# Optimization experiments

Hardware: AMD Instinct MI355X
Metric: run time of the kernel (lower is better)

Reference implementation:

```python
import jax, jax.numpy as jnp
import numpy as np

N_NODES = 100000
N_EDGES = 800000
D_MODEL = 128


def setup_inputs() -> dict:
    key = jax.random.key(0)
    ks = jax.random.split(key, 8)
    nodes = jax.random.normal(ks[0], (N_NODES, D_MODEL), dtype=jnp.float32)
    senders = jax.random.randint(ks[1], (N_EDGES,), 0, N_NODES)
    receivers = jax.random.randint(ks[2], (N_EDGES,), 0, N_NODES)
    edges = jax.random.uniform(ks[3], (N_EDGES,), dtype=jnp.float32)
    W1 = jax.random.normal(ks[4], (D_MODEL, D_MODEL), dtype=jnp.float32) / np.sqrt(D_MODEL)
    b1 = jnp.zeros((D_MODEL,), dtype=jnp.float32)
    W2 = jax.random.normal(ks[5], (D_MODEL, D_MODEL), dtype=jnp.float32) / np.sqrt(D_MODEL)
    b2 = jnp.zeros((D_MODEL,), dtype=jnp.float32)
    return {"nodes": nodes, "senders": senders, "receivers": receivers,
            "edges": edges, "W1": W1, "b1": b1, "W2": W2, "b2": b2}


def _gcn_conv(x, s, r, e, W, b):
    # GCNConv (add_self_loops=False): linear transform, symmetric degree
    # normalization by edge weights, scatter-add aggregation at receivers.
    x = x @ W  # [N, d]
    deg = jax.ops.segment_sum(e, r, num_segments=N_NODES)  # weighted in-degree [N]
    dis = jnp.where(deg > 0, jax.lax.rsqrt(jnp.where(deg > 0, deg, 1.0)), 0.0)
    w = dis[s] * e * dis[r]  # normalized edge weight [E]
    msg = x[s] * w[:, None]  # gather + scale, [E, d] (dominant HBM traffic)
    out = jax.ops.segment_sum(msg, r, num_segments=N_NODES)  # scatter-add [N, d]
    return out + b


def reference(nodes, senders, receivers, edges, W1, b1, W2, b2):
    # to_undirected: duplicate every edge in both directions
    s = jnp.concatenate([senders, receivers])
    r = jnp.concatenate([receivers, senders])
    e = jnp.concatenate([edges, edges])
    # k_hop = 2 with residual (tightening_factor == 1), no activation, no norm
    nodes = nodes + _gcn_conv(nodes, s, r, e, W1, b1)
    nodes = nodes + _gcn_conv(nodes, s, r, e, W2, b2)
    return nodes
```

## Files before the change

### kernel.cpp

```cpp
#include <hip/hip_runtime.h>
#include <hip/hip_bf16.h>

#define D 128

typedef __attribute__((ext_vector_type(8))) short bf16x8;
typedef __attribute__((ext_vector_type(4))) float f32x4;

static __device__ __forceinline__ short f2bf(float f) {
  __hip_bfloat16 h = __float2bfloat16(f);
  return *reinterpret_cast<short*>(&h);
}

__global__ __launch_bounds__(256) void k_degcnt(
    const int* __restrict__ s, const int* __restrict__ r,
    const float* __restrict__ e, float* __restrict__ deg,
    int* __restrict__ cnt, int E) {
  int i = blockIdx.x * 256 + threadIdx.x;
  if (i < E) {
    int sv = s[i], rv = r[i];
    float ev = e[i];
    atomicAdd(&deg[rv], ev);
    atomicAdd(&deg[sv], ev);
    atomicAdd(&cnt[rv], 1);
    atomicAdd(&cnt[sv], 1);
  }
}

__global__ __launch_bounds__(256) void k_dis(float* __restrict__ deg, int N) {
  int i = blockIdx.x * 256 + threadIdx.x;
  if (i < N) {
    float d = deg[i];
    deg[i] = d > 0.f ? rsqrtf(d) : 0.f;
  }
}

__global__ __launch_bounds__(256) void k_scan1(
    const int* __restrict__ cnt, int* __restrict__ rowptr,
    int* __restrict__ chsum, int N) {
  __shared__ int ts[256];
  int tid = threadIdx.x;
  int base = blockIdx.x * 2048 + tid * 8;
  int v[8];
  int run = 0;
#pragma unroll
  for (int j = 0; j < 8; ++j) {
    int idx = base + j;
    int t = (idx < N) ? cnt[idx] : 0;
    v[j] = run;
    run += t;
  }
  ts[tid] = run;
  __syncthreads();
  for (int off = 1; off < 256; off <<= 1) {
    int t = (tid >= off) ? ts[tid - off] : 0;
    __syncthreads();
    ts[tid] += t;
    __syncthreads();
  }
  int excl = ts[tid] - run;
#pragma unroll
  for (int j = 0; j < 8; ++j) {
    int idx = base + j;
    if (idx < N) rowptr[idx] = excl + v[j];
  }
  if (tid == 255) chsum[blockIdx.x] = ts[255];
}

__global__ __launch_bounds__(64) void k_scan2(int* __restrict__ chsum, int nch) {
  if (threadIdx.x == 0) {
    int run = 0;
    for (int i = 0; i < nch; ++i) { int t = chsum[i]; chsum[i] = run; run += t; }
    chsum[nch] = run;
  }
}

__global__ __launch_bounds__(256) void k_scan3(
    int* __restrict__ rowptr, int* __restrict__ cursor,
    const int* __restrict__ chsum, int N, int nch) {
  int i = blockIdx.x * 256 + threadIdx.x;
  if (i < N) {
    int v = rowptr[i] + chsum[i >> 11];
    rowptr[i] = v;
    cursor[i] = v;
  } else if (i == N) {
    rowptr[N] = chsum[nch];
  }
}

__global__ __launch_bounds__(256) void k_fill(
    const int* __restrict__ s, const int* __restrict__ r,
    const float* __restrict__ e, const float* __restrict__ dis,
    int* __restrict__ cursor, int2* __restrict__ ent, int E) {
  int i = blockIdx.x * 256 + threadIdx.x;
  if (i >= E) return;
  int sv = s[i], rv = r[i];
  float w = dis[sv] * e[i] * dis[rv];
  int wy = __float_as_int(w);
  int p1 = atomicAdd(&cursor[rv], 1);
  ent[p1] = make_int2(sv, wy);
  int p2 = atomicAdd(&cursor[sv], 1);
  ent[p2] = make_int2(rv, wy);
}

__global__ __launch_bounds__(256) void k_wprep2(
    const float* __restrict__ W1, const float* __restrict__ W2,
    unsigned short* __restrict__ Wt1, unsigned short* __restrict__ Wt2) {
  int idx = blockIdx.x * 256 + threadIdx.x;
  const float* W = (idx < D * D) ? W1 : W2;
  unsigned short* Wt = (idx < D * D) ? Wt1 : Wt2;
  int t = idx & (D * D - 1);
  int col = t >> 7, k = t & 127;
  Wt[t] = (unsigned short)f2bf(W[k * D + col]);
}

__global__ __launch_bounds__(256) void k_gemm_mfma(
    const float* __restrict__ X, const unsigned short* __restrict__ Wt,
    unsigned short* __restrict__ Y, int nrows) {
  __shared__ unsigned short wl[128 * 128];
  int tid = threadIdx.x;
  {
    const int4* src = reinterpret_cast<const int4*>(Wt);
#pragma unroll
    for (int j = 0; j < 8; ++j) {
      int c = tid + 256 * j;
      int4 v = src[c];
      int byte = c * 16;
      int col = byte >> 8;
      int swz = byte ^ ((col & 7) << 4);
      *reinterpret_cast<int4*>(reinterpret_cast<char*>(wl) + swz) = v;
    }
  }
  __syncthreads();

  int lane = tid & 63;
  int wv = tid >> 6;
  int lr = lane & 15;
  int kgrp = lane >> 4;
  int row = blockIdx.x * 64 + wv * 16 + lr;
  bool valid = row < nrows;

  f32x4 acc[8];
#pragma unroll
  for (int n = 0; n < 8; ++n) acc[n] = (f32x4){0.f, 0.f, 0.f, 0.f};

#pragma unroll
  for (int ks = 0; ks < 4; ++ks) {
    bf16x8 a;
    if (valid) {
      const float4* xp = reinterpret_cast<const float4*>(
          X + (size_t)row * D + ks * 32 + kgrp * 8);
      float4 f0 = xp[0], f1 = xp[1];
      a[0] = f2bf(f0.x); a[1] = f2bf(f0.y); a[2] = f2bf(f0.z); a[3] = f2bf(f0.w);
      a[4] = f2bf(f1.x); a[5] = f2bf(f1.y); a[6] = f2bf(f1.z); a[7] = f2bf(f1.w);
    } else {
      a = (bf16x8){0, 0, 0, 0, 0, 0, 0, 0};
    }
#pragma unroll
    for (int n = 0; n < 8; ++n) {
      int col = n * 16 + lr;
      int byte = col * 256 + ks * 64 + kgrp * 16;
      int swz = byte ^ ((col & 7) << 4);
      bf16x8 b = *reinterpret_cast<const bf16x8*>(
          reinterpret_cast<const char*>(wl) + swz);
      acc[n] = __builtin_amdgcn_mfma_f32_16x16x32_bf16(a, b, acc[n], 0, 0, 0);
    }
  }

  int r0 = blockIdx.x * 64 + wv * 16 + kgrp * 4;
#pragma unroll
  for (int n = 0; n < 8; ++n) {
    int col = n * 16 + lr;
#pragma unroll
    for (int i = 0; i < 4; ++i) {
      int rr = r0 + i;
      if (rr < nrows) Y[(size_t)rr * D + col] = (unsigned short)f2bf(acc[n][i]);
    }
  }
}

__global__ __launch_bounds__(256) void k_agg(
    const int* __restrict__ rowptr, const int2* __restrict__ ent,
    const unsigned int* __restrict__ X2, const float* __restrict__ prev,
    const float* __restrict__ bias, float* __restrict__ out, int N) {
  int node = blockIdx.x * 4 + (threadIdx.x >> 6);
  int lane = threadIdx.x & 63;
  if (node >= N) return;
  float2 acc = reinterpret_cast<const float2*>(prev)[(size_t)node * 64 + lane];
  float2 bb = reinterpret_cast<const float2*>(bias)[lane];
  acc.x += bb.x; acc.y += bb.y;
  int beg = rowptr[node], end = rowptr[node + 1];
  int j = beg;
  for (; j + 8 <= end; j += 8) {
    int2 ee[8];
#pragma unroll
    for (int u = 0; u < 8; ++u) ee[u] = ent[j + u];
    unsigned int xz[8];
#pragma unroll
    for (int u = 0; u < 8; ++u) xz[u] = X2[(size_t)ee[u].x * 64 + lane];
#pragma unroll
    for (int u = 0; u < 8; ++u) {
      float w = __int_as_float(ee[u].y);
      acc.x = fmaf(__uint_as_float(xz[u] << 16), w, acc.x);
      acc.y = fmaf(__uint_as_float(xz[u] & 0xffff0000u), w, acc.y);
    }
  }
  for (; j < end; ++j) {
    int2 eJ = ent[j];
    float w = __int_as_float(eJ.y);
    unsigned int xz = X2[(size_t)eJ.x * 64 + lane];
    acc.x = fmaf(__uint_as_float(xz << 16), w, acc.x);
    acc.y = fmaf(__uint_as_float(xz & 0xffff0000u), w, acc.y);
  }
  reinterpret_cast<float2*>(out)[(size_t)node * 64 + lane] = acc;
}

extern "C" void kernel_launch(void* const* d_in, const int* in_sizes, int n_in,
                              void* d_out, int out_size, void* d_ws, size_t ws_size,
                              hipStream_t stream) {
  const float* nodes     = (const float*)d_in[0];
  const int*   senders   = (const int*)d_in[1];
  const int*   receivers = (const int*)d_in[2];
  const float* edges     = (const float*)d_in[3];
  const float* W1        = (const float*)d_in[4];
  const float* b1        = (const float*)d_in[5];
  const float* W2        = (const float*)d_in[6];
  const float* b2        = (const float*)d_in[7];
  float* out = (float*)d_out;

  int N = in_sizes[0] / D;
  int E = in_sizes[1];
  int NCH = (N + 2047) / 2048;

  auto alignup = [](size_t x) { return (x + 511) / 512 * 512; };
  char* p = (char*)d_ws;
  float* deg    = (float*)p; p += alignup((size_t)N * 4);
  int*   cnt    = (int*)p;   p += alignup((size_t)N * 4);
  int*   rowptr = (int*)p;   p += alignup(((size_t)N + 1) * 4);
  int*   cursor = (int*)p;   p += alignup((size_t)N * 4);
  int*   chsum  = (int*)p;   p += alignup(((size_t)NCH + 1) * 4);
  int2*  ent    = (int2*)p;  p += alignup((size_t)2 * E * 8);
  unsigned short* Wt1 = (unsigned short*)p; p += alignup((size_t)D * D * 2);
  unsigned short* Wt2 = (unsigned short*)p; p += alignup((size_t)D * D * 2);
  unsigned short* X   = (unsigned short*)p;

  hipMemsetAsync(deg, 0, (size_t)N * 4, stream);
  hipMemsetAsync(cnt, 0, (size_t)N * 4, stream);

  int eb = (E + 255) / 256;
  k_degcnt<<<eb, 256, 0, stream>>>(senders, receivers, edges, deg, cnt, E);
  k_dis<<<(N + 255) / 256, 256, 0, stream>>>(deg, N);

  k_scan1<<<NCH, 256, 0, stream>>>(cnt, rowptr, chsum, N);
  k_scan2<<<1, 64, 0, stream>>>(chsum, NCH);
  k_scan3<<<(N + 1 + 255) / 256, 256, 0, stream>>>(rowptr, cursor, chsum, N, NCH);
  k_fill<<<eb, 256, 0, stream>>>(senders, receivers, edges, deg, cursor, ent, E);

  k_wprep2<<<(2 * D * D) / 256, 256, 0, stream>>>(W1, W2, Wt1, Wt2);

  int gemm_blocks = (N + 63) / 64;
  int agg_blocks = (N + 3) / 4;

  k_gemm_mfma<<<gemm_blocks, 256, 0, stream>>>(nodes, Wt1, X, N);
  k_agg<<<agg_blocks, 256, 0, stream>>>(rowptr, ent, (const unsigned int*)X,
                                        nodes, b1, out, N);

  k_gemm_mfma<<<gemm_blocks, 256, 0, stream>>>(out, Wt2, X, N);
  k_agg<<<agg_blocks, 256, 0, stream>>>(rowptr, ent, (const unsigned int*)X,
                                        out, b2, out, N);
}
```

Baseline: 533.5 us.

## Compute degrees from CSR rows instead of float atomics; add nontemporal hints

Removes the float atomic degree accumulation and the per-node rsqrt pass. Edges are now bucketed with their raw weights, then each node's degree is summed from its CSR row with a wave reduction, and a second per-row pass rewrites the weights into normalized form. Nontemporal loads and stores are also added for the edge streams, the CSR fill, and the aggregation prev/out rows. This trades 1.6M float atomics for two extra passes over the 12.8MB CSR. The nontemporal stores of out may also hurt reuse when the second GEMM reads that buffer.

```diff
diff --git a/kernel.cpp b/kernel.cpp
--- a/kernel.cpp
+++ b/kernel.cpp
@@ -5,32 +5,23 @@
 
 typedef __attribute__((ext_vector_type(8))) short bf16x8;
 typedef __attribute__((ext_vector_type(4))) float f32x4;
+typedef __attribute__((ext_vector_type(2))) float f32x2;
+typedef __attribute__((ext_vector_type(2))) int int2v;
 
 static __device__ __forceinline__ short f2bf(float f) {
   __hip_bfloat16 h = __float2bfloat16(f);
   return *reinterpret_cast<short*>(&h);
 }
 
-__global__ __launch_bounds__(256) void k_degcnt(
+__global__ __launch_bounds__(256) void k_cnt(
     const int* __restrict__ s, const int* __restrict__ r,
-    const float* __restrict__ e, float* __restrict__ deg,
     int* __restrict__ cnt, int E) {
   int i = blockIdx.x * 256 + threadIdx.x;
   if (i < E) {
-    int sv = s[i], rv = r[i];
-    float ev = e[i];
-    atomicAdd(&deg[rv], ev);
-    atomicAdd(&deg[sv], ev);
+    int sv = __builtin_nontemporal_load(s + i);
+    int rv = __builtin_nontemporal_load(r + i);
     atomicAdd(&cnt[rv], 1);
     atomicAdd(&cnt[sv], 1);
-  }
-}
-
-__global__ __launch_bounds__(256) void k_dis(float* __restrict__ deg, int N) {
-  int i = blockIdx.x * 256 + threadIdx.x;
-  if (i < N) {
-    float d = deg[i];
-    deg[i] = d > 0.f ? rsqrtf(d) : 0.f;
   }
 }
 
@@ -89,17 +80,51 @@
 
 __global__ __launch_bounds__(256) void k_fill(
     const int* __restrict__ s, const int* __restrict__ r,
-    const float* __restrict__ e, const float* __restrict__ dis,
-    int* __restrict__ cursor, int2* __restrict__ ent, int E) {
+    const float* __restrict__ e,
+    int* __restrict__ cursor, int2v* __restrict__ ent, int E) {
   int i = blockIdx.x * 256 + threadIdx.x;
   if (i >= E) return;
-  int sv = s[i], rv = r[i];
-  float w = dis[sv] * e[i] * dis[rv];
-  int wy = __float_as_int(w);
+  int sv = __builtin_nontemporal_load(s + i);
+  int rv = __builtin_nontemporal_load(r + i);
+  float ev = __builtin_nontemporal_load(e + i);
+  int ey = __float_as_int(ev);
   int p1 = atomicAdd(&cursor[rv], 1);
-  ent[p1] = make_int2(sv, wy);
+  int2v v1; v1.x = sv; v1.y = ey;
+  __builtin_nontemporal_store(v1, ent + p1);
   int p2 = atomicAdd(&cursor[sv], 1);
-  ent[p2] = make_int2(rv, wy);
+  int2v v2; v2.x = rv; v2.y = ey;
+  __builtin_nontemporal_store(v2, ent + p2);
+}
+
+__global__ __launch_bounds__(256) void k_degdis(
+    const int* __restrict__ rowptr, const int2v* __restrict__ ent,
+    float* __restrict__ dis, int N) {
+  int node = blockIdx.x * 4 + (threadIdx.x >> 6);
+  int lane = threadIdx.x & 63;
+  if (node >= N) return;
+  int beg = rowptr[node], end = rowptr[node + 1];
+  float sum = 0.f;
+  for (int j = beg + lane; j < end; j += 64)
+    sum += __int_as_float(ent[j].y);
+#pragma unroll
+  for (int off = 32; off; off >>= 1) sum += __shfl_xor(sum, off, 64);
+  if (lane == 0) dis[node] = sum > 0.f ? rsqrtf(sum) : 0.f;
+}
+
+__global__ __launch_bounds__(256) void k_normw(
+    const int* __restrict__ rowptr, int2v* __restrict__ ent,
+    const float* __restrict__ dis, int N) {
+  int node = blockIdx.x * 4 + (threadIdx.x >> 6);
+  int lane = threadIdx.x & 63;
+  if (node >= N) return;
+  float dself = dis[node];
+  int beg = rowptr[node], end = rowptr[node + 1];
+  for (int j = beg + lane; j < end; j += 64) {
+    int2v v = ent[j];
+    float w = dself * __int_as_float(v.y) * dis[v.x];
+    v.y = __float_as_int(w);
+    ent[j] = v;
+  }
 }
 
 __global__ __launch_bounds__(256) void k_wprep2(
@@ -179,39 +204,42 @@
 }
 
 __global__ __launch_bounds__(256) void k_agg(
-    const int* __restrict__ rowptr, const int2* __restrict__ ent,
+    const int* __restrict__ rowptr, const int2v* __restrict__ ent,
     const unsigned int* __restrict__ X2, const float* __restrict__ prev,
     const float* __restrict__ bias, float* __restrict__ out, int N) {
   int node = blockIdx.x * 4 + (threadIdx.x >> 6);
   int lane = threadIdx.x & 63;
   if (node >= N) return;
-  float2 acc = reinterpret_cast<const float2*>(prev)[(size_t)node * 64 + lane];
+  f32x2 pv = __builtin_nontemporal_load(
+      reinterpret_cast<const f32x2*>(prev) + (size_t)node * 64 + lane);
   float2 bb = reinterpret_cast<const float2*>(bias)[lane];
-  acc.x += bb.x; acc.y += bb.y;
+  float ax = pv.x + bb.x, ay = pv.y + bb.y;
   int beg = rowptr[node], end = rowptr[node + 1];
   int j = beg;
   for (; j + 8 <= end; j += 8) {
-    int2 ee[8];
-#pragma unroll
-    for (int u = 0; u < 8; ++u) ee[u] = ent[j + u];
+    int2v ee[8];
+#pragma unroll
+    for (int u = 0; u < 8; ++u) ee[u] = __builtin_nontemporal_load(ent + j + u);
     unsigned int xz[8];
 #pragma unroll
     for (int u = 0; u < 8; ++u) xz[u] = X2[(size_t)ee[u].x * 64 + lane];
 #pragma unroll
     for (int u = 0; u < 8; ++u) {
       float w = __int_as_float(ee[u].y);
-      acc.x = fmaf(__uint_as_float(xz[u] << 16), w, acc.x);
-      acc.y = fmaf(__uint_as_float(xz[u] & 0xffff0000u), w, acc.y);
+      ax = fmaf(__uint_as_float(xz[u] << 16), w, ax);
+      ay = fmaf(__uint_as_float(xz[u] & 0xffff0000u), w, ay);
     }
   }
   for (; j < end; ++j) {
-    int2 eJ = ent[j];
+    int2v eJ = ent[j];
     float w = __int_as_float(eJ.y);
     unsigned int xz = X2[(size_t)eJ.x * 64 + lane];
-    acc.x = fmaf(__uint_as_float(xz << 16), w, acc.x);
-    acc.y = fmaf(__uint_as_float(xz & 0xffff0000u), w, acc.y);
-  }
-  reinterpret_cast<float2*>(out)[(size_t)node * 64 + lane] = acc;
+    ax = fmaf(__uint_as_float(xz << 16), w, ax);
+    ay = fmaf(__uint_as_float(xz & 0xffff0000u), w, ay);
+  }
+  f32x2 res; res.x = ax; res.y = ay;
+  __builtin_nontemporal_store(
+      res, reinterpret_cast<f32x2*>(out) + (size_t)node * 64 + lane);
 }
 
 extern "C" void kernel_launch(void* const* d_in, const int* in_sizes, int n_in,
@@ -233,38 +261,39 @@
 
   auto alignup = [](size_t x) { return (x + 511) / 512 * 512; };
   char* p = (char*)d_ws;
-  float* deg    = (float*)p; p += alignup((size_t)N * 4);
+  float* dis    = (float*)p; p += alignup((size_t)N * 4);
   int*   cnt    = (int*)p;   p += alignup((size_t)N * 4);
   int*   rowptr = (int*)p;   p += alignup(((size_t)N + 1) * 4);
   int*   cursor = (int*)p;   p += alignup((size_t)N * 4);
   int*   chsum  = (int*)p;   p += alignup(((size_t)NCH + 1) * 4);
-  int2*  ent    = (int2*)p;  p += alignup((size_t)2 * E * 8);
+  int2v* ent    = (int2v*)p; p += alignup((size_t)2 * E * 8);
   unsigned short* Wt1 = (unsigned short*)p; p += alignup((size_t)D * D * 2);
   unsigned short* Wt2 = (unsigned short*)p; p += alignup((size_t)D * D * 2);
   unsigned short* X   = (unsigned short*)p;
 
-  hipMemsetAsync(deg, 0, (size_t)N * 4, stream);
   hipMemsetAsync(cnt, 0, (size_t)N * 4, stream);
 
   int eb = (E + 255) / 256;
-  k_degcnt<<<eb, 256, 0, stream>>>(senders, receivers, edges, deg, cnt, E);
-  k_dis<<<(N + 255) / 256, 256, 0, stream>>>(deg, N);
-
+  int nb4 = (N + 3) / 4;
+
+  k_cnt<<<eb, 256, 0, stream>>>(senders, receivers, cnt, E);
   k_scan1<<<NCH, 256, 0, stream>>>(cnt, rowptr, chsum, N);
   k_scan2<<<1, 64, 0, stream>>>(chsum, NCH);
   k_scan3<<<(N + 1 + 255) / 256, 256, 0, stream>>>(rowptr, cursor, chsum, N, NCH);
-  k_fill<<<eb, 256, 0, stream>>>(senders, receivers, edges, deg, cursor, ent, E);
+  k_fill<<<eb, 256, 0, stream>>>(senders, receivers, edges, cursor, ent, E);
+
+  k_degdis<<<nb4, 256, 0, stream>>>(rowptr, ent, dis, N);
+  k_normw<<<nb4, 256, 0, stream>>>(rowptr, ent, dis, N);
 
   k_wprep2<<<(2 * D * D) / 256, 256, 0, stream>>>(W1, W2, Wt1, Wt2);
 
   int gemm_blocks = (N + 63) / 64;
-  int agg_blocks = (N + 3) / 4;
 
   k_gemm_mfma<<<gemm_blocks, 256, 0, stream>>>(nodes, Wt1, X, N);
-  k_agg<<<agg_blocks, 256, 0, stream>>>(rowptr, ent, (const unsigned int*)X,
-                                        nodes, b1, out, N);
+  k_agg<<<nb4, 256, 0, stream>>>(rowptr, ent, (const unsigned int*)X,
+                                 nodes, b1, out, N);
 
   k_gemm_mfma<<<gemm_blocks, 256, 0, stream>>>(out, Wt2, X, N);
-  k_agg<<<agg_blocks, 256, 0, stream>>>(rowptr, ent, (const unsigned int*)X,
-                                        out, b2, out, N);
-}
+  k_agg<<<nb4, 256, 0, stream>>>(rowptr, ent, (const unsigned int*)X,
+                                 out, b2, out, N);
+}
```

Result: slower. 560.6 us (+5.1%).
